# Kernel optimization log

Measured on AMD Instinct MI355X. Metric: run time of the kernel, lower is better.

The kernel has to match this reference:

```python
import jax, jax.numpy as jnp
import numpy as np

N = 50000      # nodes
E = 800000     # edges (avg degree 16)
IN = 128       # in_channels
OUT = 2        # out_channels
HID = 100 * OUT  # MAX_CHANNELS * out_channels = 200
MSG_EPS = 1e-7   # GENConv message eps
BN_EPS = 1e-5    # BatchNorm1d eps


def _gen_conv(x, src, dst, w1, b1, g, be, w2, b2):
    """PyG GENConv with defaults: aggr='softmax', t=1.0, msg_norm=False,
    MLP=[c, 2c, c_out] with BatchNorm1d+ReLU between layers (train-mode BN)."""
    # message: relu(x_j) + eps  -> [E, d]
    msg = jnp.maximum(x[src], 0.0) + MSG_EPS
    # scatter softmax over incoming edges of each destination node (t=1)
    m = jax.ops.segment_max(msg, dst, num_segments=N)          # [N, d]
    m = jnp.where(jnp.isfinite(m), m, 0.0)                      # isolated nodes
    ex = jnp.exp(msg - m[dst])                                  # [E, d]
    s = jax.ops.segment_sum(ex, dst, num_segments=N)            # [N, d]
    alpha = ex / (s[dst] + 1e-16)                               # [E, d]
    out = jax.ops.segment_sum(msg * alpha, dst, num_segments=N) # [N, d]
    out = out + x                                               # residual with x_dst
    # MLP: Linear -> BatchNorm(batch stats) -> ReLU -> Linear
    h = out @ w1 + b1                                           # [N, 2d]
    mu = h.mean(axis=0)
    var = h.var(axis=0)
    h = (h - mu) * jax.lax.rsqrt(var + BN_EPS) * g + be
    h = jnp.maximum(h, 0.0)
    return h @ w2 + b2


def setup_inputs() -> dict:
    key = jax.random.key(0)
    ks = jax.random.split(key, 8)
    rn = lambda k, shp, s: jax.random.normal(k, shp, jnp.float32) * s
    mid1, mid2 = 2 * IN, 2 * HID
    return {
        "x": rn(ks[0], (N, IN), 1.0),
        "edge_index": jax.random.randint(ks[1], (2, E), 0, N, jnp.int32),
        "c1_w1": rn(ks[2], (IN, mid1), 0.05), "c1_b1": jnp.zeros((mid1,), jnp.float32),
        "c1_g": jnp.ones((mid1,), jnp.float32), "c1_beta": jnp.zeros((mid1,), jnp.float32),
        "c1_w2": rn(ks[3], (mid1, HID), 0.05), "c1_b2": jnp.zeros((HID,), jnp.float32),
        "c2_w1": rn(ks[4], (HID, mid2), 0.05), "c2_b1": jnp.zeros((mid2,), jnp.float32),
        "c2_g": jnp.ones((mid2,), jnp.float32), "c2_beta": jnp.zeros((mid2,), jnp.float32),
        "c2_w2": rn(ks[5], (mid2, OUT), 0.05), "c2_b2": jnp.zeros((OUT,), jnp.float32),
    }


def reference(x, edge_index, c1_w1, c1_b1, c1_g, c1_beta, c1_w2, c1_b2,
              c2_w1, c2_b1, c2_g, c2_beta, c2_w2, c2_b2):
    src, dst = edge_index[0], edge_index[1]
    h = jnp.maximum(_gen_conv(x, src, dst, c1_w1, c1_b1, c1_g, c1_beta, c1_w2, c1_b2), 0.0)
    # Dropout(p=0.1) is identity in eval mode (deterministic reference)
    return jnp.maximum(_gen_conv(h, src, dst, c2_w1, c2_b1, c2_g, c2_beta, c2_w2, c2_b2), 0.0)
```

## Files before the change

kernel.cpp:

```cpp
#include <hip/hip_runtime.h>
#include <hip/hip_bf16.h>
#include <stdint.h>

#define NNODES 50000
#define NEDGES 800000
#define DIN 128
#define DHID 200
#define MID1 256
#define MID2 400
#define SCAN_NB ((NNODES + 255) / 256)
#define NBB ((NNODES + 127) / 128)
#define RSPLIT 12
#define LOG2E 1.4426950408889634f
#define LN2 0.6931471805599453f
#define GK_SPLIT 96
#define GCH 208
#define GNP 40
#define NBUCK 98
#define BCAP 16384
#define EPB 4096

typedef __hip_bfloat16 bf16;
typedef __attribute__((ext_vector_type(8))) short short8;
typedef __attribute__((ext_vector_type(4))) float floatx4;
typedef unsigned short ushort;

__device__ __forceinline__ float b2f(bf16 v) { return __bfloat162float(v); }
__device__ __forceinline__ bf16 f2b(float v) { return __float2bfloat16(v); }
__device__ __forceinline__ float bits2f(ushort b) {
    unsigned u = ((unsigned)b) << 16;
    return __uint_as_float(u);
}
__device__ __forceinline__ ushort f2bits(float f) {
    bf16 h = __float2bfloat16(f);
    return *(ushort*)&h;
}
__device__ __forceinline__ float ldin(const void* p, size_t i, int f32) {
    return f32 ? ((const float*)p)[i] : __bfloat162float(((const bf16*)p)[i]);
}
__device__ __forceinline__ void ldin4(const void* p, size_t i, int f32, float* v) {
    if (f32) {
        float4 f = *(const float4*)((const float*)p + i);
        v[0] = f.x; v[1] = f.y; v[2] = f.z; v[3] = f.w;
    } else {
        ushort4 u = *(const ushort4*)((const bf16*)p + i);
        v[0] = bits2f(u.x); v[1] = bits2f(u.y); v[2] = bits2f(u.z); v[3] = bits2f(u.w);
    }
}
__device__ __forceinline__ float fexp2(float x) {
#if __has_builtin(__builtin_amdgcn_exp2f)
    return __builtin_amdgcn_exp2f(x);
#else
    return exp2f(x);
#endif
}
__device__ __forceinline__ floatx4 mfma16(short8 a, short8 b, floatx4 c) {
    return __builtin_amdgcn_mfma_f32_16x16x32_bf16(a, b, c, 0, 0, 0);
}
__device__ __forceinline__ void acc4(ushort4 u, float* s, float* p) {
    ushort uu[4];
    *(ushort4*)uu = u;
#pragma unroll
    for (int c = 0; c < 4; c++) {
        float v = bits2f(uu[c]);
        float ee = fexp2(v);
        s[c] += ee;
        p[c] = fmaf(v, ee, p[c]);
    }
}

__global__ __launch_bounds__(256) void bin_kernel(const int* __restrict__ src,
                                                  const int* __restrict__ dst,
                                                  const void* __restrict__ g,
                                                  int* __restrict__ flag,
                                                  unsigned* __restrict__ bbuf,
                                                  int* __restrict__ gcur) {
    __shared__ int cnt[NBUCK], cur[NBUCK];
    int tid = threadIdx.x;
    if (blockIdx.x == 0 && tid == 0)
        *flag = (((const unsigned*)g)[0] == 0x3F800000u) ? 1 : 0;
    if (tid < NBUCK) cnt[tid] = 0;
    __syncthreads();
    int e0 = blockIdx.x * EPB;
    unsigned pk[16];
    int bk[16];
#pragma unroll
    for (int i = 0; i < 16; i++) {
        int e = e0 + i * 256 + tid;
        if (e < NEDGES) {
            int d = dst[e], s = src[e];
            pk[i] = ((unsigned)d << 16) | (unsigned)s;
            bk[i] = d >> 9;
            atomicAdd(&cnt[bk[i]], 1);
        } else {
            bk[i] = -1;
        }
    }
    __syncthreads();
    if (tid < NBUCK) cur[tid] = atomicAdd(&gcur[tid], cnt[tid]);
    __syncthreads();
#pragma unroll
    for (int i = 0; i < 16; i++) {
        if (bk[i] >= 0) {
            int off = atomicAdd(&cur[bk[i]], 1);
            bbuf[(size_t)bk[i] * BCAP + off] = pk[i];
        }
    }
}

__global__ __launch_bounds__(256) void histb_kernel(const unsigned* __restrict__ bbuf,
                                                    const int* __restrict__ gcur,
                                                    int* __restrict__ counts) {
    __shared__ int hc[512];
    int b = blockIdx.x, tid = threadIdx.x;
    int base = b << 9;
    int nn = min(512, NNODES - base);
    for (int i = tid; i < 512; i += 256) hc[i] = 0;
    __syncthreads();
    int cnt = gcur[b];
    const unsigned* eb = bbuf + (size_t)b * BCAP;
    for (int i = tid; i < cnt; i += 256) atomicAdd(&hc[(eb[i] >> 16) - base], 1);
    __syncthreads();
    for (int i = tid; i < nn; i += 256) counts[base + i] = hc[i];
}

__global__ __launch_bounds__(512) void scatterb_kernel(const unsigned* __restrict__ bbuf,
                                                       const int* __restrict__ gcur,
                                                       const int* __restrict__ rowptr,
                                                       int* __restrict__ ssrc) {
    __shared__ int lc[512];
    int b = blockIdx.x, tid = threadIdx.x;
    int base = b << 9;
    int nn = min(512, NNODES - base);
    lc[tid] = (tid < nn) ? rowptr[base + tid] : 0;
    __syncthreads();
    int cnt = gcur[b];
    const unsigned* eb = bbuf + (size_t)b * BCAP;
    for (int i = tid; i < cnt; i += 512) {
        unsigned p = eb[i];
        int node = (int)(p >> 16) - base;
        int idx = atomicAdd(&lc[node], 1);
        ssrc[idx] = (int)(p & 0xFFFFu);
    }
}

__global__ __launch_bounds__(256) void scanA_kernel(const int* __restrict__ counts,
                                                    int* __restrict__ rowptr,
                                                    int* __restrict__ blocksums) {
    __shared__ int sh[256];
    int t = threadIdx.x, b = blockIdx.x;
    int i = b * 256 + t;
    int v = (i < NNODES) ? counts[i] : 0;
    sh[t] = v;
    __syncthreads();
#pragma unroll
    for (int off = 1; off < 256; off <<= 1) {
        int o = (t >= off) ? sh[t - off] : 0;
        __syncthreads();
        sh[t] += o;
        __syncthreads();
    }
    if (i < NNODES) rowptr[i] = sh[t] - v;
    if (t == 255) blocksums[b] = sh[255];
}

__global__ __launch_bounds__(256) void scanC_kernel(int* __restrict__ rowptr,
                                                    const int* __restrict__ blocksums) {
    __shared__ int sh[256];
    int t = threadIdx.x, b = blockIdx.x;
    sh[t] = (t < SCAN_NB) ? blocksums[t] : 0;
    __syncthreads();
#pragma unroll
    for (int off = 1; off < 256; off <<= 1) {
        int o = (t >= off) ? sh[t - off] : 0;
        __syncthreads();
        sh[t] += o;
        __syncthreads();
    }
    int boff = (b > 0) ? sh[b - 1] : 0;
    int i = b * 256 + t;
    if (i < NNODES) rowptr[i] += boff;
    if (i == 0) rowptr[NNODES] = NEDGES;
}

#define TW (DIN * MID1 + MID1 * DHID + DHID * MID2)
__global__ __launch_bounds__(256) void prep_kernel(const void* __restrict__ W1, bf16* __restrict__ Wt1,
                                                   const void* __restrict__ W2, bf16* __restrict__ Wt2,
                                                   const void* __restrict__ W3, bf16* __restrict__ Wt3,
                                                   const void* __restrict__ X, bf16* __restrict__ M1,
                                                   ushort* __restrict__ dummy,
                                                   const int* __restrict__ flag) {
    const int S1 = DIN * MID1, S2 = MID1 * DHID;
    int f32 = *flag;
    int idx = blockIdx.x * 256 + threadIdx.x;
    if (idx < TW) {
        const void* W;
        bf16* Wt;
        int K, N, li;
        if (idx < S1) { W = W1; Wt = Wt1; K = DIN; N = MID1; li = idx; }
        else if (idx < S1 + S2) { W = W2; Wt = Wt2; K = MID1; N = DHID; li = idx - S1; }
        else { W = W3; Wt = Wt3; K = DHID; N = MID2; li = idx - S1 - S2; }
        int k = li / N, n = li - k * N;
        Wt[(size_t)n * K + k] = f2b(ldin(W, li, f32));
    }
    if (idx < DHID) dummy[idx] = 0xC300;
    int i = idx * 4;
    if (i < NNODES * DIN) {
        float v[4];
        ldin4(X, i, f32, v);
        ushort4 o;
        o.x = f2bits((fmaxf(v[0], 0.f) + 1e-7f) * LOG2E);
        o.y = f2bits((fmaxf(v[1], 0.f) + 1e-7f) * LOG2E);
        o.z = f2bits((fmaxf(v[2], 0.f) + 1e-7f) * LOG2E);
        o.w = f2bits((fmaxf(v[3], 0.f) + 1e-7f) * LOG2E);
        int node = i >> 7, c = i & 127;
        int s = c >> 5, c2 = c & 31;
        *(ushort4*)(M1 + (size_t)s * 1600000 + (size_t)node * 32 + c2) = o;
    }
}

__global__ __launch_bounds__(256) void agg1_kernel(const void* __restrict__ X,
                                                   const bf16* __restrict__ M1,
                                                   const int* __restrict__ rowptr,
                                                   const int* __restrict__ ssrc,
                                                   const ushort* __restrict__ dummy,
                                                   const int* __restrict__ flag,
                                                   bf16* __restrict__ out) {
    int f32 = *flag;
    int tid = threadIdx.x;
    int w = tid >> 6, lane = tid & 63;
    int g = lane >> 3, k = lane & 7;
    int bx = blockIdx.x;
    int xs = bx & 7;
    int s = xs >> 1;
    int ni = (bx >> 3) * 2 + (xs & 1);
    int n = ni * 4 + w;
    int r0 = __builtin_amdgcn_readfirstlane(rowptr[n]);
    int deg = __builtin_amdgcn_readfirstlane(rowptr[n + 1]) - r0;
    const char* base = (const char*)M1 + (size_t)s * 3200000;
    const char* dm = (const char*)dummy + k * 8;
    float sa[4] = {0.f, 0.f, 0.f, 0.f}, pa[4] = {0.f, 0.f, 0.f, 0.f};
    for (int i = 0; i < deg; i += 16) {
        int e0 = i + g, e1 = i + 8 + g;
        bool v0 = e0 < deg, v1 = e1 < deg;
        int i0 = ssrc[r0 + (v0 ? e0 : 0)];
        int i1 = ssrc[r0 + (v1 ? e1 : 0)];
        const char* p0 = v0 ? base + (size_t)(unsigned)i0 * 64u + k * 8 : dm;
        const char* p1 = v1 ? base + (size_t)(unsigned)i1 * 64u + k * 8 : dm;
        ushort4 u0 = *(const ushort4*)p0;
        ushort4 u1 = *(const ushort4*)p1;
        acc4(u0, sa, pa);
        acc4(u1, sa, pa);
    }
#pragma unroll
    for (int d = 8; d < 64; d <<= 1) {
#pragma unroll
        for (int c = 0; c < 4; c++) {
            sa[c] += __shfl_xor(sa[c], d, 64);
            pa[c] += __shfl_xor(pa[c], d, 64);
        }
    }
    if (g == 0) {
        int c0 = s * 32 + k * 4;
        float xc[4];
        ldin4(X, (size_t)n * DIN + c0, f32, xc);
        ushort4 o;
        o.x = f2bits(fmaf(LN2, pa[0] / (sa[0] + 1e-16f), xc[0]));
        o.y = f2bits(fmaf(LN2, pa[1] / (sa[1] + 1e-16f), xc[1]));
        o.z = f2bits(fmaf(LN2, pa[2] / (sa[2] + 1e-16f), xc[2]));
        o.w = f2bits(fmaf(LN2, pa[3] / (sa[3] + 1e-16f), xc[3]));
        *(ushort4*)(out + (size_t)n * DIN + c0) = o;
    }
}

__global__ __launch_bounds__(256) void agg2_kernel(const bf16* __restrict__ M2,
                                                   const int* __restrict__ rowptr,
                                                   const int* __restrict__ ssrc,
                                                   const ushort* __restrict__ dummy,
                                                   bf16* __restrict__ out) {
    int lane = threadIdx.x & 63;
    int n = blockIdx.x * 4 + (threadIdx.x >> 6);
    int r0 = __builtin_amdgcn_readfirstlane(rowptr[n]);
    int deg = __builtin_amdgcn_readfirstlane(rowptr[n + 1]) - r0;
    bool act = lane < 50;
    int boff = (act ? lane : 49) << 3;
    const char* M2b = (const char*)M2;
    const char* dp = (const char*)dummy;
    float s[4] = {0.f, 0.f, 0.f, 0.f}, p[4] = {0.f, 0.f, 0.f, 0.f};
    int nfull = deg >> 3;
    for (int b = 0; b < nfull; b++) {
        const int* ep = ssrc + r0 + (b << 3);
        ushort4 u[8];
#pragma unroll
        for (int k = 0; k < 8; k++)
            u[k] = *(const ushort4*)(M2b + (size_t)((unsigned)ep[k] * 400u) + boff);
#pragma unroll
        for (int k = 0; k < 8; k++) acc4(u[k], s, p);
    }
    int rem = deg & 7;
    if (rem) {
        const int* ep = ssrc + r0 + (nfull << 3);
        ushort4 u[8];
#pragma unroll
        for (int k = 0; k < 8; k++) {
            const char* rp = (k < rem) ? (M2b + (size_t)((unsigned)ep[k] * 400u)) : dp;
            u[k] = *(const ushort4*)(rp + boff);
        }
#pragma unroll
        for (int k = 0; k < 8; k++) acc4(u[k], s, p);
    }
    if (act) {
        ushort4 u = *(const ushort4*)(M2b + (size_t)n * 400 + boff);
        float vn[4] = {bits2f(u.x), bits2f(u.y), bits2f(u.z), bits2f(u.w)};
        ushort4 o;
        o.x = f2bits(LN2 * (p[0] / (s[0] + 1e-16f) + vn[0]) - 1e-7f);
        o.y = f2bits(LN2 * (p[1] / (s[1] + 1e-16f) + vn[1]) - 1e-7f);
        o.z = f2bits(LN2 * (p[2] / (s[2] + 1e-16f) + vn[2]) - 1e-7f);
        o.w = f2bits(LN2 * (p[3] / (s[3] + 1e-16f) + vn[3]) - 1e-7f);
        *(ushort4*)(out + (size_t)n * DHID + 4 * lane) = o;
    }
}

template <int MODE, int NT, int KK, int NCOL>
__global__ __launch_bounds__(512, 4) void bgemm(const bf16* __restrict__ A,
                                                const bf16* __restrict__ Bt,
                                                const void* __restrict__ bias,
                                                const int* __restrict__ flag,
                                                const float* __restrict__ sc,
                                                const float* __restrict__ offs,
                                                const void* __restrict__ w2,
                                                bf16* __restrict__ Out, int ostride,
                                                float* __restrict__ psum,
                                                float* __restrict__ psq,
                                                float* __restrict__ fscr, int M) {
    constexpr int KP = (KK + 31) & ~31;
    constexpr int KS = KP / 32;
    constexpr int KV8 = KP / 8;
    __shared__ short Bs[NT * 16][KP + 8];
    int f32 = *flag;
    int tid = threadIdx.x;
    int cb = blockIdx.y * NCOL;

    for (int idx = tid; idx < NT * 16 * KV8; idx += 512) {
        int col = idx / KV8, kq = (idx - col * KV8) * 8;
        uint4 v = {0, 0, 0, 0};
        if (col < NCOL && kq < KK) v = *(const uint4*)(Bt + (size_t)(cb + col) * KK + kq);
        *(uint4*)&Bs[col][kq] = v;
    }
    __syncthreads();

    int w = tid >> 6, L = tid & 63;
    int lm = L & 15, q = L >> 4;
    int rw = blockIdx.x * 128 + w * 16;
    int ar = rw + lm;
    bool rok = ar < M;

    uint4 af[KS];
#pragma unroll
    for (int s = 0; s < KS; s++) {
        int k = s * 32 + q * 8;
        af[s] = (uint4){0, 0, 0, 0};
        if (rok && k + 8 <= KK) af[s] = *(const uint4*)(A + (size_t)ar * KK + k);
    }

    floatx4 acc[NT];
#pragma unroll
    for (int t = 0; t < NT; t++) acc[t] = (floatx4){0.f, 0.f, 0.f, 0.f};

#pragma unroll
    for (int s = 0; s < KS; s++) {
        short8 as;
        if (MODE == 1) {
            int ch = s * 32 + q * 8;
            float4 sA = *(const float4*)(sc + ch), sB = *(const float4*)(sc + ch + 4);
            float4 oA = *(const float4*)(offs + ch), oB = *(const float4*)(offs + ch + 4);
            float scv[8] = {sA.x, sA.y, sA.z, sA.w, sB.x, sB.y, sB.z, sB.w};
            float ofv[8] = {oA.x, oA.y, oA.z, oA.w, oB.x, oB.y, oB.z, oB.w};
            ushort us[8];
            *(uint4*)us = af[s];
#pragma unroll
            for (int j = 0; j < 8; j++)
                us[j] = f2bits(fmaxf(fmaf(bits2f(us[j]), scv[j], ofv[j]), 0.f));
            as = *(short8*)us;
        } else {
            as = *(short8*)&af[s];
        }
#pragma unroll
        for (int t = 0; t < NT; t++) {
            short8 bf = *(const short8*)&Bs[t * 16 + lm][s * 32 + q * 8];
            acc[t] = mfma16(as, bf, acc[t]);
        }
    }

    if (MODE == 0) {
#pragma unroll
        for (int t = 0; t < NT; t++) {
            int col = t * 16 + lm;
            float bb = ldin(bias, col, f32);
            float cs = 0.f, cq = 0.f;
#pragma unroll
            for (int r = 0; r < 4; r++) {
                int gm = rw + q * 4 + r;
                if (gm < M) {
                    float v = acc[t][r] + bb;
                    Out[(size_t)gm * ostride + col] = f2b(v);
                    cs += v;
                    cq += v * v;
                }
            }
            cs += __shfl_xor(cs, 16, 64); cq += __shfl_xor(cq, 16, 64);
            cs += __shfl_xor(cs, 32, 64); cq += __shfl_xor(cq, 32, 64);
            if (q == 0) {
                psum[(size_t)(blockIdx.x * 8 + w) * (NT * 16) + col] = cs;
                psq[(size_t)(blockIdx.x * 8 + w) * (NT * 16) + col] = cq;
            }
        }
    }
    if (MODE == 1) {
#pragma unroll
        for (int t = 0; t < NT; t++) {
            int col = t * 16 + lm;
            if (col < NCOL) {
                int gg = cb + col;
                float bb = ldin(bias, gg, f32);
#pragma unroll
                for (int r = 0; r < 4; r++) {
                    int gm = rw + q * 4 + r;
                    if (gm < M) {
                        float v = acc[t][r] + bb;
                        Out[(size_t)gm * ostride + gg] = f2b((fmaxf(v, 0.f) + 1e-7f) * LOG2E);
                    }
                }
            }
        }
    }
    if (MODE == 2) {
        float s0[4] = {0.f, 0.f, 0.f, 0.f}, s1[4] = {0.f, 0.f, 0.f, 0.f};
#pragma unroll
        for (int t = 0; t < NT; t++) {
            int col = t * 16 + lm;
            if (col < NCOL) {
                int gg = cb + col;
                float bb = ldin(bias, gg, f32);
                float scv = sc[gg], ofv = offs[gg];
                float w20 = ldin(w2, 2 * gg, f32), w21 = ldin(w2, 2 * gg + 1, f32);
#pragma unroll
                for (int r = 0; r < 4; r++) {
                    float vn = fmaxf((acc[t][r] + bb) * scv + ofv, 0.f);
                    s0[r] = fmaf(vn, w20, s0[r]);
                    s1[r] = fmaf(vn, w21, s1[r]);
                }
            }
        }
#pragma unroll
        for (int d = 1; d < 16; d <<= 1) {
#pragma unroll
            for (int r = 0; r < 4; r++) {
                s0[r] += __shfl_xor(s0[r], d, 64);
                s1[r] += __shfl_xor(s1[r], d, 64);
            }
        }
        if (lm == 0) {
#pragma unroll
            for (int r = 0; r < 4; r++) {
                int gm = rw + q * 4 + r;
                if (gm < M) {
                    fscr[(size_t)gm * 8 + blockIdx.y * 2 + 0] = s0[r];
                    fscr[(size_t)gm * 8 + blockIdx.y * 2 + 1] = s1[r];
                }
            }
        }
    }
}

__global__ __launch_bounds__(256) void stats_reduce(const float* __restrict__ psum,
                                                    const float* __restrict__ psq,
                                                    float* __restrict__ bnsum,
                                                    float* __restrict__ bnsumsq,
                                                    int NB, int NC) {
    __shared__ float shs[4][64], shq[4][64];
    int cc = threadIdx.x & 63;
    int c = blockIdx.x * 64 + cc;
    int ro = threadIdx.x >> 6;
    int chunk = (NB + RSPLIT - 1) / RSPLIT;
    int b0 = blockIdx.y * chunk;
    int b1 = min(b0 + chunk, NB);
    float s = 0.f, sq = 0.f;
    if (c < NC) {
        for (int b = b0 + ro; b < b1; b += 4) {
            s += psum[(size_t)b * NC + c];
            sq += psq[(size_t)b * NC + c];
        }
    }
    shs[ro][cc] = s;
    shq[ro][cc] = sq;
    __syncthreads();
    if (threadIdx.x < 64) {
        int gc = blockIdx.x * 64 + threadIdx.x;
        if (gc < NC) {
            int t = threadIdx.x;
            float ts = shs[0][t] + shs[1][t] + shs[2][t] + shs[3][t];
            float tq = shq[0][t] + shq[1][t] + shq[2][t] + shq[3][t];
            atomicAdd(&bnsum[gc], ts);
            atomicAdd(&bnsumsq[gc], tq);
        }
    }
}

__global__ void bn_finish(const float* __restrict__ sum, const float* __restrict__ sumsq,
                          const void* __restrict__ g, const void* __restrict__ be,
                          const int* __restrict__ flag,
                          float* __restrict__ sc, float* __restrict__ off, int C) {
    int f32 = *flag;
    int c = blockIdx.x * blockDim.x + threadIdx.x;
    if (c < C) {
        float mu = sum[c] / (float)NNODES;
        float var = fmaxf(sumsq[c] / (float)NNODES - mu * mu, 0.f);
        float rstd = rsqrtf(var + 1e-5f);
        float s = rstd * ldin(g, c, f32);
        sc[c] = s;
        off[c] = ldin(be, c, f32) - mu * s;
    }
}

__global__ __launch_bounds__(512) void gram_kernel(const bf16* __restrict__ X,
                                                   float* __restrict__ pg) {
    __shared__ short T[GCH][GNP];
    int tid = threadIdx.x;
    int w = tid >> 6, L = tid & 63;
    int lm = L & 15, q = L >> 4;
    floatx4 acc[2][13];
#pragma unroll
    for (int c = 0; c < 2; c++)
#pragma unroll
        for (int t = 0; t < 13; t++) acc[c][t] = (floatx4){0.f, 0.f, 0.f, 0.f};

    const int chunks = (NNODES + 32 * GK_SPLIT - 1) / (32 * GK_SPLIT);
    int base0 = blockIdx.x * chunks * 32;
    for (int ch = 0; ch < chunks; ch++) {
        int nb = base0 + ch * 32;
#pragma unroll
        for (int p = 0; p < 4; p++) {
            int idx = tid + p * 512;
            if (idx < 1600) {
                int nl = idx & 31, cq = idx >> 5;
                int gn = nb + nl;
                ushort4 u = {0, 0, 0, 0};
                if (gn < NNODES) u = *(const ushort4*)(X + (size_t)gn * DHID + cq * 4);
                T[cq * 4 + 0][nl] = (short)u.x;
                T[cq * 4 + 1][nl] = (short)u.y;
                T[cq * 4 + 2][nl] = (short)u.z;
                T[cq * 4 + 3][nl] = (short)u.w;
            }
        }
        if (tid < 256) {
            int nl = tid & 31, c = 200 + (tid >> 5);
            int gn = nb + nl;
            T[c][nl] = (c == 200 && gn < NNODES) ? (short)0x3F80 : (short)0;
        }
        __syncthreads();
        short8 af[13];
#pragma unroll
        for (int t = 0; t < 13; t++) af[t] = *(const short8*)&T[t * 16 + lm][q * 8];
#pragma unroll
        for (int c = 0; c < 2; c++) {
            int cj = w + c * 8;
            if (cj < 13) {
                short8 bf = *(const short8*)&T[cj * 16 + lm][q * 8];
#pragma unroll
                for (int t = 0; t < 13; t++) acc[c][t] = mfma16(af[t], bf, acc[c][t]);
            }
        }
        __syncthreads();
    }
    float* pgb = pg + (size_t)blockIdx.x * (GCH * GCH);
#pragma unroll
    for (int c = 0; c < 2; c++) {
        int cj = w + c * 8;
        if (cj < 13) {
#pragma unroll
            for (int t = 0; t < 13; t++)
#pragma unroll
                for (int r = 0; r < 4; r++)
                    pgb[(size_t)(t * 16 + q * 4 + r) * GCH + cj * 16 + lm] = acc[c][t][r];
        }
    }
}

__global__ void greduce_kernel(const float* __restrict__ pg, float* __restrict__ G) {
    int e = blockIdx.x * 256 + threadIdx.x;
    if (e < GCH * GCH) {
        float s = 0.f;
        for (int b = 0; b < GK_SPLIT; b++) s += pg[(size_t)b * (GCH * GCH) + e];
        G[e] = s;
    }
}

__global__ __launch_bounds__(256) void bn2_finish(const float* __restrict__ G,
                                                  const bf16* __restrict__ Wt3,
                                                  const void* __restrict__ b1,
                                                  const void* __restrict__ g,
                                                  const void* __restrict__ be,
                                                  const int* __restrict__ flag,
                                                  float* __restrict__ sc,
                                                  float* __restrict__ off) {
    __shared__ float wl[200];
    __shared__ float red[256];
    __shared__ float dsh;
    int f32 = *flag;
    int c = blockIdx.x;
    int t = threadIdx.x;
    if (t < 200) wl[t] = b2f(Wt3[(size_t)c * DHID + t]);
    __syncthreads();
    float di = 0.f;
    if (t <= 200) {
        const float* Gr = G + (size_t)t * GCH;
        for (int j = 0; j < 200; j++) di = fmaf(Gr[j], wl[j], di);
    }
    red[t] = (t < 200) ? wl[t] * di : 0.f;
    if (t == 200) dsh = di;
    __syncthreads();
    for (int o = 128; o > 0; o >>= 1) {
        if (t < o) red[t] += red[t + o];
        __syncthreads();
    }
    if (t == 0) {
        float d = dsh;
        float bc = ldin(b1, c, f32);
        float mu = d / (float)NNODES + bc;
        float eh2 = (red[0] + 2.f * bc * d) / (float)NNODES + bc * bc;
        float var = fmaxf(eh2 - mu * mu, 0.f);
        float rstd = rsqrtf(var + 1e-5f);
        float s = rstd * ldin(g, c, f32);
        sc[c] = s;
        off[c] = ldin(be, c, f32) - mu * s;
    }
}

__global__ void final_combine(const float* __restrict__ fscr, const void* __restrict__ b2,
                              const int* __restrict__ flag, void* __restrict__ outp, int M) {
    int f32 = *flag;
    int n = blockIdx.x * 256 + threadIdx.x;
    if (n < M) {
        const float* f = fscr + (size_t)n * 8;
        float v0 = fmaxf(f[0] + f[2] + f[4] + f[6] + ldin(b2, 0, f32), 0.f);
        float v1 = fmaxf(f[1] + f[3] + f[5] + f[7] + ldin(b2, 1, f32), 0.f);
        if (f32) {
            ((float*)outp)[2 * n] = v0;
            ((float*)outp)[2 * n + 1] = v1;
        } else {
            ((bf16*)outp)[2 * n] = f2b(v0);
            ((bf16*)outp)[2 * n + 1] = f2b(v1);
        }
    }
}

extern "C" void kernel_launch(void* const* d_in, const int* in_sizes, int n_in,
                              void* d_out, int out_size, void* d_ws, size_t ws_size,
                              hipStream_t stream) {
    const void* x = d_in[0];
    const int* ei = (const int*)d_in[1];
    const void* c1_w1 = d_in[2];
    const void* c1_b1 = d_in[3];
    const void* c1_g = d_in[4];
    const void* c1_be = d_in[5];
    const void* c1_w2 = d_in[6];
    const void* c1_b2 = d_in[7];
    const void* c2_w1 = d_in[8];
    const void* c2_b1 = d_in[9];
    const void* c2_g = d_in[10];
    const void* c2_be = d_in[11];
    const void* c2_w2 = d_in[12];
    const void* c2_b2 = d_in[13];

    const int* src = ei;
    const int* dst = ei + NEDGES;

    uint8_t* w = (uint8_t*)d_ws;
    int* rowptr = (int*)(w + 0);
    int* counts = (int*)(w + 204800);
    bf16* wT1 = (bf16*)(w + 204800);
    bf16* wT2 = (bf16*)(w + 270336);
    bf16* wT3 = (bf16*)(w + 409600);
    int* ssrc = (int*)(w + 614400);
    float* bnbuf = (float*)(w + 3814400);
    float* sum1 = bnbuf, *sumsq1 = bnbuf + 256;
    int* gcur = (int*)(bnbuf + 512);
    float* sc1 = bnbuf + 1312, *off1 = bnbuf + 1568;
    float* sc2 = bnbuf + 1824, *off2 = bnbuf + 2224;
    int* flag_in = (int*)(bnbuf + 2624);
    int* blocksums = (int*)(bnbuf + 2640);
    ushort* dummyrow = (ushort*)(bnbuf + 2840);
    uint8_t* bufA = w + 3830784;
    uint8_t* bufB = w + 23830784;
    unsigned* bbuf = (unsigned*)bufA;
    bf16* out1 = (bf16*)bufA;
    bf16* h1 = (bf16*)bufA;
    float* fscr = (float*)bufA;
    float* pg = (float*)bufA;
    float* Gm = (float*)(bufA + 17000000);
    bf16* M1 = (bf16*)bufB;
    bf16* t1 = (bf16*)bufB;
    bf16* out2 = (bf16*)bufB;
    float* ps1 = (float*)(bufA + 12800000);
    float* pq1 = ps1 + (size_t)NBB * 8 * MID1;

    hipMemsetAsync(bnbuf, 0, 1312 * sizeof(float), stream);

    bin_kernel<<<(NEDGES + EPB - 1) / EPB, 256, 0, stream>>>(src, dst, c1_g, flag_in,
                                                             bbuf, gcur);
    histb_kernel<<<NBUCK, 256, 0, stream>>>(bbuf, gcur, counts);
    scanA_kernel<<<SCAN_NB, 256, 0, stream>>>(counts, rowptr, blocksums);
    scanC_kernel<<<SCAN_NB, 256, 0, stream>>>(rowptr, blocksums);
    scatterb_kernel<<<NBUCK, 512, 0, stream>>>(bbuf, gcur, rowptr, ssrc);

    prep_kernel<<<(NNODES * DIN / 4 + 255) / 256, 256, 0, stream>>>(
        c1_w1, wT1, c1_w2, wT2, c2_w1, wT3, x, M1, dummyrow, flag_in);

    agg1_kernel<<<50000, 256, 0, stream>>>(x, M1, rowptr, ssrc, dummyrow, flag_in, out1);
    bgemm<0, 16, 128, 256><<<dim3(NBB, 1), 512, 0, stream>>>(
        out1, wT1, c1_b1, flag_in, nullptr, nullptr, nullptr,
        t1, MID1, ps1, pq1, nullptr, NNODES);
    stats_reduce<<<dim3((MID1 + 63) / 64, RSPLIT), 256, 0, stream>>>(ps1, pq1, sum1, sumsq1,
                                                                     NBB * 8, MID1);
    bn_finish<<<1, 256, 0, stream>>>(sum1, sumsq1, c1_g, c1_be, flag_in, sc1, off1, MID1);
    bgemm<1, 7, 256, 100><<<dim3(NBB, 2), 512, 0, stream>>>(
        t1, wT2, c1_b2, flag_in, sc1, off1, nullptr,
        h1, DHID, nullptr, nullptr, nullptr, NNODES);

    agg2_kernel<<<NNODES / 4, 256, 0, stream>>>(h1, rowptr, ssrc, dummyrow, out2);
    gram_kernel<<<GK_SPLIT, 512, 0, stream>>>(out2, pg);
    greduce_kernel<<<(GCH * GCH + 255) / 256, 256, 0, stream>>>(pg, Gm);
    bn2_finish<<<MID2, 256, 0, stream>>>(Gm, wT3, c2_b1, c2_g, c2_be, flag_in, sc2, off2);
    bgemm<2, 7, 200, 100><<<dim3(NBB, 4), 512, 0, stream>>>(
        out2, wT3, c2_b1, flag_in, sc2, off2, c2_w2,
        nullptr, 0, nullptr, nullptr, fscr, NNODES);
    final_combine<<<(NNODES + 255) / 256, 256, 0, stream>>>(fscr, c2_b2, flag_in,
                                                            d_out, NNODES);
}
```

Baseline: 412.8 us.

## Sort nodes by degree and assign one node per 8-lane group in agg1

Adds a counting sort of nodes by in-degree (histogram, scan, scatter kernels) and restructures agg1 so each 8-lane group handles one node instead of a whole wave per node. Lanes in a group share edge indices via shuffles, and the wave loops until all its groups finish. Degree sorting keeps the groups in a wave balanced. A padded sentinel row in M1 replaces the separate dummy buffer for out-of-range edges. This cuts the cross-lane reductions and the idle lanes of the old mapping, at the cost of three extra small kernels and indirect node indexing.

```diff
diff --git a/kernel.cpp b/kernel.cpp
--- a/kernel.cpp
+++ b/kernel.cpp
@@ -19,6 +19,8 @@
 #define NBUCK 98
 #define BCAP 16384
 #define EPB 4096
+#define M1_STRIDE 1600032
+#define M1_STRIDE_B 3200064
 
 typedef __hip_bfloat16 bf16;
 typedef __attribute__((ext_vector_type(8))) short short8;
@@ -181,6 +183,53 @@
     int i = b * 256 + t;
     if (i < NNODES) rowptr[i] += boff;
     if (i == 0) rowptr[NNODES] = NEDGES;
+}
+
+__global__ __launch_bounds__(256) void dhist_kernel(const int* __restrict__ counts,
+                                                    int* __restrict__ dh) {
+    __shared__ int lh[128];
+    int tid = threadIdx.x;
+    if (tid < 128) lh[tid] = 0;
+    __syncthreads();
+    int i = blockIdx.x * 256 + tid;
+    if (i < NNODES) atomicAdd(&lh[min(counts[i], 127)], 1);
+    __syncthreads();
+    if (tid < 128 && lh[tid] > 0) atomicAdd(&dh[tid], lh[tid]);
+}
+
+__global__ __launch_bounds__(128) void dscan_kernel(const int* __restrict__ dh,
+                                                    int* __restrict__ dcur) {
+    __shared__ int sh[128];
+    int t = threadIdx.x;
+    sh[t] = dh[t];
+    __syncthreads();
+#pragma unroll
+    for (int off = 1; off < 128; off <<= 1) {
+        int o = (t >= off) ? sh[t - off] : 0;
+        __syncthreads();
+        sh[t] += o;
+        __syncthreads();
+    }
+    dcur[t] = sh[t] - dh[t];
+}
+
+__global__ __launch_bounds__(256) void dscatter_kernel(const int* __restrict__ counts,
+                                                       int* __restrict__ dcur,
+                                                       int* __restrict__ nodeorder) {
+    __shared__ int lh[128], lo[128];
+    int tid = threadIdx.x;
+    if (tid < 128) lh[tid] = 0;
+    __syncthreads();
+    int i = blockIdx.x * 256 + tid;
+    int b = -1, my = 0;
+    if (i < NNODES) {
+        b = min(counts[i], 127);
+        my = atomicAdd(&lh[b], 1);
+    }
+    __syncthreads();
+    if (tid < 128 && lh[tid] > 0) lo[tid] = atomicAdd(&dcur[tid], lh[tid]);
+    __syncthreads();
+    if (b >= 0) nodeorder[lo[b] + my] = i;
 }
 
 #define TW (DIN * MID1 + MID1 * DHID + DHID * MID2)
@@ -204,6 +253,10 @@
         Wt[(size_t)n * K + k] = f2b(ldin(W, li, f32));
     }
     if (idx < DHID) dummy[idx] = 0xC300;
+    if (idx < 128) {
+        int sl = idx >> 5, c2 = idx & 31;
+        ((ushort*)M1)[(size_t)sl * M1_STRIDE + (size_t)NNODES * 32 + c2] = 0xC300;
+    }
     int i = idx * 4;
     if (i < NNODES * DIN) {
         float v[4];
@@ -215,7 +268,7 @@
         o.w = f2bits((fmaxf(v[3], 0.f) + 1e-7f) * LOG2E);
         int node = i >> 7, c = i & 127;
         int s = c >> 5, c2 = c & 31;
-        *(ushort4*)(M1 + (size_t)s * 1600000 + (size_t)node * 32 + c2) = o;
+        *(ushort4*)(M1 + (size_t)s * M1_STRIDE + (size_t)node * 32 + c2) = o;
     }
 }
 
@@ -223,7 +276,7 @@
                                                    const bf16* __restrict__ M1,
                                                    const int* __restrict__ rowptr,
                                                    const int* __restrict__ ssrc,
-                                                   const ushort* __restrict__ dummy,
+                                                   const int* __restrict__ nodeorder,
                                                    const int* __restrict__ flag,
                                                    bf16* __restrict__ out) {
     int f32 = *flag;
@@ -233,34 +286,30 @@
     int bx = blockIdx.x;
     int xs = bx & 7;
     int s = xs >> 1;
-    int ni = (bx >> 3) * 2 + (xs & 1);
-    int n = ni * 4 + w;
-    int r0 = __builtin_amdgcn_readfirstlane(rowptr[n]);
-    int deg = __builtin_amdgcn_readfirstlane(rowptr[n + 1]) - r0;
-    const char* base = (const char*)M1 + (size_t)s * 3200000;
-    const char* dm = (const char*)dummy + k * 8;
+    int half = xs & 1;
+    int bi = bx >> 3;
+    int pos = (((bi * 2 + half) * 4 + w) << 3) + g;
+    bool valid = pos < NNODES;
+    int n = valid ? nodeorder[pos] : 0;
+    int r0 = rowptr[n];
+    int deg = valid ? rowptr[n + 1] - r0 : 0;
+    const char* base = (const char*)M1 + (size_t)s * M1_STRIDE_B;
+    int k8 = k * 8;
     float sa[4] = {0.f, 0.f, 0.f, 0.f}, pa[4] = {0.f, 0.f, 0.f, 0.f};
-    for (int i = 0; i < deg; i += 16) {
-        int e0 = i + g, e1 = i + 8 + g;
-        bool v0 = e0 < deg, v1 = e1 < deg;
-        int i0 = ssrc[r0 + (v0 ? e0 : 0)];
-        int i1 = ssrc[r0 + (v1 ? e1 : 0)];
-        const char* p0 = v0 ? base + (size_t)(unsigned)i0 * 64u + k * 8 : dm;
-        const char* p1 = v1 ? base + (size_t)(unsigned)i1 * 64u + k * 8 : dm;
-        ushort4 u0 = *(const ushort4*)p0;
-        ushort4 u1 = *(const ushort4*)p1;
-        acc4(u0, sa, pa);
-        acc4(u1, sa, pa);
-    }
-#pragma unroll
-    for (int d = 8; d < 64; d <<= 1) {
-#pragma unroll
-        for (int c = 0; c < 4; c++) {
-            sa[c] += __shfl_xor(sa[c], d, 64);
-            pa[c] += __shfl_xor(pa[c], d, 64);
-        }
-    }
-    if (g == 0) {
+    for (int i = 0;; i += 8) {
+        if (__all(i >= deg)) break;
+        int e = ssrc[(i + k < deg) ? r0 + i + k : 0];
+        ushort4 u[8];
+#pragma unroll
+        for (int j = 0; j < 8; j++) {
+            int ej = __shfl(e, j, 8);
+            int row = (i + j < deg) ? ej : NNODES;
+            u[j] = *(const ushort4*)(base + (size_t)(unsigned)row * 64u + k8);
+        }
+#pragma unroll
+        for (int j = 0; j < 8; j++) acc4(u[j], sa, pa);
+    }
+    if (valid) {
         int c0 = s * 32 + k * 4;
         float xc[4];
         ldin4(X, (size_t)n * DIN + c0, f32, xc);
@@ -686,6 +735,8 @@
     float* bnbuf = (float*)(w + 3814400);
     float* sum1 = bnbuf, *sumsq1 = bnbuf + 256;
     int* gcur = (int*)(bnbuf + 512);
+    int* dh = (int*)(bnbuf + 640);
+    int* dcur = (int*)(bnbuf + 768);
     float* sc1 = bnbuf + 1312, *off1 = bnbuf + 1568;
     float* sc2 = bnbuf + 1824, *off2 = bnbuf + 2224;
     int* flag_in = (int*)(bnbuf + 2624);
@@ -704,6 +755,7 @@
     bf16* out2 = (bf16*)bufB;
     float* ps1 = (float*)(bufA + 12800000);
     float* pq1 = ps1 + (size_t)NBB * 8 * MID1;
+    int* nodeorder = (int*)(bufA + 19400000);
 
     hipMemsetAsync(bnbuf, 0, 1312 * sizeof(float), stream);
 
@@ -714,10 +766,14 @@
     scanC_kernel<<<SCAN_NB, 256, 0, stream>>>(rowptr, blocksums);
     scatterb_kernel<<<NBUCK, 512, 0, stream>>>(bbuf, gcur, rowptr, ssrc);
 
+    dhist_kernel<<<SCAN_NB, 256, 0, stream>>>(counts, dh);
+    dscan_kernel<<<1, 128, 0, stream>>>(dh, dcur);
+    dscatter_kernel<<<SCAN_NB, 256, 0, stream>>>(counts, dcur, nodeorder);
+
     prep_kernel<<<(NNODES * DIN / 4 + 255) / 256, 256, 0, stream>>>(
         c1_w1, wT1, c1_w2, wT2, c2_w1, wT3, x, M1, dummyrow, flag_in);
 
-    agg1_kernel<<<50000, 256, 0, stream>>>(x, M1, rowptr, ssrc, dummyrow, flag_in, out1);
+    agg1_kernel<<<6256, 256, 0, stream>>>(x, M1, rowptr, ssrc, nodeorder, flag_in, out1);
     bgemm<0, 16, 128, 256><<<dim3(NBB, 1), 512, 0, stream>>>(
         out1, wT1, c1_b1, flag_in, nullptr, nullptr, nullptr,
         t1, MID1, ps1, pq1, nullptr, NNODES);
```

After: 384.5 us. 1.07x faster.
